# Optimization experiments

Measured on AMD Instinct MI355X. Metric: run time of the kernel, lower is better.

The kernel has to match this reference:

```python
import jax, jax.numpy as jnp
import numpy as np

IN, OUT, B = 2048, 1000, 8192
EXP = (2048, 4096, 6144, 8192)
LN_EPS = 1e-5


def _mish(v):
    return v * jnp.tanh(jax.nn.softplus(v))


def _gelu(v):
    return jax.nn.gelu(v, approximate=False)  # torch F.gelu default is exact erf


def setup_inputs() -> dict:
    key = jax.random.key(0)
    ks = iter(jax.random.split(key, 48))
    nk = lambda: next(ks)
    r = lambda shape, s=0.02: jax.random.normal(nk(), shape, jnp.float32) * s
    d = {"x": jax.random.normal(nk(), (B, IN), jnp.float32)}
    d["W"] = r((OUT, IN), 0.05)
    d["b"] = r((OUT,), 0.01)
    for i, e in enumerate(EXP):
        d[f"up_w{i}"] = r((e, IN))
        d[f"down_w{i}"] = r((OUT, e))
        d[f"router_w{i}"] = r((i + 2, IN), 0.05)
        d[f"router_b{i}"] = r((i + 2,), 0.01)
    d["scales"] = r((4,), 0.1)
    d["ln_g"] = jnp.ones((IN,), jnp.float32)
    d["ln_b"] = jnp.zeros((IN,), jnp.float32)
    d["dom_router_w"] = r((4, IN), 0.05)
    d["dom_router_b"] = r((4,), 0.01)
    d["dom_experts_w"] = r((OUT * 4, IN))
    d["calib_w"] = r((OUT, IN))
    d["calib_b"] = r((OUT,), 0.01)
    d["rg_w1"] = r((IN // 4, IN))
    d["rg_w2"] = r((OUT, IN // 4))
    d["rg_b2"] = r((OUT,), 0.01)
    d["zeta"] = jnp.float32(0.5)
    d["theta"] = jnp.float32(0.5)
    d["lambda_"] = jnp.float32(0.5)
    return d


def _forward(x, W, b,
             up_w0, down_w0, router_w0, router_b0,
             up_w1, down_w1, router_w1, router_b1,
             up_w2, down_w2, router_w2, router_b2,
             up_w3, down_w3, router_w3, router_b3,
             scales, ln_g, ln_b,
             dom_router_w, dom_router_b, dom_experts_w,
             calib_w, calib_b, rg_w1, rg_w2, rg_b2,
             zeta, theta, lambda_):
    acts = (jax.nn.silu, _gelu, _mish, jax.nn.relu)
    ups = (up_w0, up_w1, up_w2, up_w3)
    downs = (down_w0, down_w1, down_w2, down_w3)
    r_ws = (router_w0, router_w1, router_w2, router_w3)
    r_bs = (router_b0, router_b1, router_b2, router_b3)

    base_logits = x @ W.T + b                      # [B, OUT]
    # dropout is identity (eval mode)
    branch_outs = [acts[i](x @ ups[i].T) @ downs[i].T for i in range(4)]  # each [B, OUT]

    final_mix = base_logits
    for i in range(4):
        route = jax.nn.softmax(x @ r_ws[i].T + r_bs[i], axis=-1)  # [B, i+2]
        # only first i+1 routing weights are used (faithful to source)
        mix = sum(route[..., j:j + 1] * branch_outs[j] for j in range(i + 1))
        final_mix = final_mix + scales[i] * mix

    # pre_norm (LayerNorm, eps=1e-5)
    mu = jnp.mean(x, axis=-1, keepdims=True)
    var = jnp.var(x, axis=-1, keepdims=True)
    h = (x - mu) * jax.lax.rsqrt(var + LN_EPS) * ln_g + ln_b

    dom_logits = (jax.nn.silu(h) @ dom_experts_w.T).reshape(h.shape[0], 4, OUT)
    dom_w = jax.nn.softmax(h @ dom_router_w.T + dom_router_b, axis=-1)[..., None]  # [B,4,1]
    dom_mix = jnp.sum(dom_w * dom_logits, axis=-2)                                 # [B,OUT]

    calib = jnp.tanh(h @ calib_w.T + calib_b)
    reason = jnp.tanh(jax.nn.silu(x @ rg_w1.T) @ rg_w2.T + rg_b2)
    return final_mix + zeta * dom_mix + theta * calib + lambda_ * reason


def reference(x, W, b,
              up_w0, down_w0, router_w0, router_b0,
              up_w1, down_w1, router_w1, router_b1,
              up_w2, down_w2, router_w2, router_b2,
              up_w3, down_w3, router_w3, router_b3,
              scales, ln_g, ln_b,
              dom_router_w, dom_router_b, dom_experts_w,
              calib_w, calib_b, rg_w1, rg_w2, rg_b2,
              zeta, theta, lambda_):
    return _forward(x, W, b,
                    up_w0, down_w0, router_w0, router_b0,
                    up_w1, down_w1, router_w1, router_b1,
                    up_w2, down_w2, router_w2, router_b2,
                    up_w3, down_w3, router_w3, router_b3,
                    scales, ln_g, ln_b,
                    dom_router_w, dom_router_b, dom_experts_w,
                    calib_w, calib_b, rg_w1, rg_w2, rg_b2,
                    zeta, theta, lambda_)
```

## Files before the change

kernel.cpp:

```cpp
#include <hip/hip_runtime.h>
#include <hip/hip_bf16.h>
#include <cstdint>
#include <cstddef>

#define DEVI __device__ __forceinline__

typedef short bf16x8 __attribute__((ext_vector_type(8)));
typedef float f32x4 __attribute__((ext_vector_type(4)));

static constexpr int B_ = 8192;
static constexpr int IN_ = 2048;
static constexpr int OUT_ = 1000;

DEVI float bf2f(unsigned short u) { return __uint_as_float(((unsigned int)u) << 16); }
DEVI unsigned short f2bf(float f) {
    unsigned int x = __float_as_uint(f);
    unsigned int r = x + 0x7FFFu + ((x >> 16) & 1u);
    return (unsigned short)(r >> 16);
}

DEVI void gload16(const unsigned short* g, unsigned short* l) {
    __builtin_amdgcn_global_load_lds((const __attribute__((address_space(1))) void*)g,
                                     (__attribute__((address_space(3))) void*)l, 16, 0, 0);
}

DEVI void xcd_swizzle(int& bx, int& by) {
    const int NX = gridDim.x, NY = gridDim.y;
    if ((NY & 7) == 0) {
        const int NYc = NY >> 3;
        const int d = by * NX + bx;
        const int xcd = d & 7, idx = d >> 3;
        by = xcd * NYc + (idx % NYc);
        bx = idx / NYc;
    }
}

DEVI float fast_tanh(float x) {
    float xc = fminf(fmaxf(x, -10.f), 10.f);
    float e = __expf(2.f * xc);
    return 1.f - 2.f / (e + 1.f);
}

template <int ACT> DEVI float apply_act(float v) {
    if constexpr (ACT == 1) return v / (1.f + __expf(-v));
    else if constexpr (ACT == 2) return 0.5f * v * (1.f + erff(v * 0.70710678118654752f));
    else if constexpr (ACT == 3) {
        float p = __expf(fminf(v, 20.f));
        float sp = (v > 20.f) ? v : __logf(1.f + p);
        return v * fast_tanh(sp);
    } else if constexpr (ACT == 4) return fmaxf(v, 0.f);
    else if constexpr (ACT == 5) return fast_tanh(v);
    else return v;
}

__global__ __launch_bounds__(256) void cvt_kernel(const float* __restrict__ in,
                                                  unsigned short* __restrict__ out, int n4) {
    int stride = gridDim.x * blockDim.x;
    for (int i = blockIdx.x * blockDim.x + threadIdx.x; i < n4; i += stride) {
        float4 v = ((const float4*)in)[i];
        ushort4 o;
        o.x = f2bf(v.x); o.y = f2bf(v.y); o.z = f2bf(v.z); o.w = f2bf(v.w);
        ((ushort4*)out)[i] = o;
    }
}

__global__ __launch_bounds__(256) void cvt_dom_kernel(const float* __restrict__ in,
                                                      unsigned short* __restrict__ out) {
    const int total = 4096 * (IN_ / 4);
    int stride = gridDim.x * blockDim.x;
    for (int i = blockIdx.x * blockDim.x + threadIdx.x; i < total; i += stride) {
        int orow = i >> 9;
        int oc4 = i & 511;
        int s = orow >> 10, r = orow & 1023;
        ushort4 o = {0, 0, 0, 0};
        if (r < 1000) {
            float4 v = ((const float4*)(in + ((size_t)(s * 1000 + r)) * IN_))[oc4];
            o.x = f2bf(v.x); o.y = f2bf(v.y); o.z = f2bf(v.z); o.w = f2bf(v.w);
        }
        ((ushort4*)out)[i] = o;
    }
}

__global__ __launch_bounds__(256) void stats_kernel(const float* __restrict__ x,
                                                    const float* __restrict__ g,
                                                    const float* __restrict__ bta,
                                                    float* __restrict__ mu,
                                                    float* __restrict__ rstd,
                                                    unsigned short* __restrict__ xb,
                                                    unsigned short* __restrict__ hb,
                                                    unsigned short* __restrict__ shb,
                                                    const int wX, const int wH, const int wS) {
    const int r = blockIdx.x;
    const int t = threadIdx.x;
    const float* xr = x + (size_t)r * IN_;
    float v[8];
    float s = 0.f, q = 0.f;
#pragma unroll
    for (int i = 0; i < 8; ++i) {
        v[i] = xr[t + i * 256];
        s += v[i];
        q += v[i] * v[i];
    }
#pragma unroll
    for (int off = 32; off > 0; off >>= 1) {
        s += __shfl_down(s, off);
        q += __shfl_down(q, off);
    }
    __shared__ float ss[4], qq[4];
    if ((t & 63) == 0) { ss[t >> 6] = s; qq[t >> 6] = q; }
    __syncthreads();
    s = ss[0] + ss[1] + ss[2] + ss[3];
    q = qq[0] + qq[1] + qq[2] + qq[3];
    const float mean = s * (1.f / IN_);
    const float var = q * (1.f / IN_) - mean * mean;
    const float rs = rsqrtf(var + 1e-5f);
    if (t == 0) { mu[r] = mean; rstd[r] = rs; }
#pragma unroll
    for (int i = 0; i < 8; ++i) {
        int c = t + i * 256;
        if (wX) xb[(size_t)r * IN_ + c] = f2bf(v[i]);
        if (wH | wS) {
            float h = (v[i] - mean) * rs * g[c] + bta[c];
            if (wH) hb[(size_t)r * IN_ + c] = f2bf(h);
            if (wS) shb[(size_t)r * IN_ + c] = f2bf(h / (1.f + __expf(-h)));
        }
    }
}

__global__ __launch_bounds__(256) void router_kernel(
    const float* __restrict__ x, const float* __restrict__ mu, const float* __restrict__ rstd,
    const float* __restrict__ g, const float* __restrict__ bta,
    const float* __restrict__ rw0, const float* __restrict__ rb0,
    const float* __restrict__ rw1, const float* __restrict__ rb1,
    const float* __restrict__ rw2, const float* __restrict__ rb2,
    const float* __restrict__ rw3, const float* __restrict__ rb3,
    const float* __restrict__ scales, const float* __restrict__ domw,
    const float* __restrict__ domb, float* __restrict__ coeff) {
    const int r = blockIdx.x;
    const int t = threadIdx.x;
    __shared__ float xs[IN_];
    __shared__ float hs[IN_];
    __shared__ float dots[18];
    const float m = mu[r], rs = rstd[r];
#pragma unroll
    for (int i = 0; i < 8; ++i) {
        int c = t + i * 256;
        float xv = x[(size_t)r * IN_ + c];
        xs[c] = xv;
        hs[c] = (xv - m) * rs * g[c] + bta[c];
    }
    __syncthreads();
    const int w = t >> 6, l = t & 63;
    const float* wp[5] = {rw0, rw1, rw2, rw3, domw};
    for (int d = w; d < 18; d += 4) {
        int gidx, row;
        if (d < 2) { gidx = 0; row = d; }
        else if (d < 5) { gidx = 1; row = d - 2; }
        else if (d < 9) { gidx = 2; row = d - 5; }
        else if (d < 14) { gidx = 3; row = d - 9; }
        else { gidx = 4; row = d - 14; }
        const float* wt = wp[gidx] + (size_t)row * IN_;
        const float* src = (gidx == 4) ? hs : xs;
        float p = 0.f;
        for (int i = l; i < IN_; i += 64) p += src[i] * wt[i];
#pragma unroll
        for (int off = 32; off > 0; off >>= 1) p += __shfl_down(p, off);
        if (l == 0) dots[d] = p;
    }
    __syncthreads();
    if (t == 0) {
        const float* rbs[4] = {rb0, rb1, rb2, rb3};
        float c[4] = {0.f, 0.f, 0.f, 0.f};
        int off = 0;
        for (int i = 0; i < 4; ++i) {
            int n = i + 2;
            float lg[5], mx = -1e30f;
            for (int j = 0; j < n; ++j) { lg[j] = dots[off + j] + rbs[i][j]; mx = fmaxf(mx, lg[j]); }
            float den = 0.f;
            for (int j = 0; j < n; ++j) { lg[j] = expf(lg[j] - mx); den += lg[j]; }
            float inv = 1.f / den;
            float sci = scales[i];
            for (int j = 0; j <= i; ++j) c[j] += sci * lg[j] * inv;
            off += n;
        }
        float dl[4], mx = -1e30f;
        for (int k = 0; k < 4; ++k) { dl[k] = dots[14 + k] + domb[k]; mx = fmaxf(mx, dl[k]); }
        float den = 0.f;
        for (int k = 0; k < 4; ++k) { dl[k] = expf(dl[k] - mx); den += dl[k]; }
        float inv = 1.f / den;
        for (int j = 0; j < 4; ++j) coeff[(size_t)r * 8 + j] = c[j];
        for (int k = 0; k < 4; ++k) coeff[(size_t)r * 8 + 4 + k] = dl[k] * inv;
    }
}

__global__ __launch_bounds__(256) void dom_reduce(
    const unsigned short* __restrict__ U, const float* __restrict__ coeff,
    float* __restrict__ out, const float* __restrict__ zetap) {
    const float zeta = zetap[0];
    const int nGroups = B_ * (OUT_ / 8);
    const int stride = gridDim.x * blockDim.x;
    for (int i = blockIdx.x * blockDim.x + threadIdx.x; i < nGroups; i += stride) {
        const int r = i / 125;
        const int c8 = (i - r * 125) * 8;
        const float w0 = zeta * coeff[(size_t)r * 8 + 4];
        const float w1 = zeta * coeff[(size_t)r * 8 + 5];
        const float w2 = zeta * coeff[(size_t)r * 8 + 6];
        const float w3 = zeta * coeff[(size_t)r * 8 + 7];
        const unsigned short* ur = U + (size_t)r * 4096 + c8;
        bf16x8 p0 = *(const bf16x8*)(ur);
        bf16x8 p1 = *(const bf16x8*)(ur + 1024);
        bf16x8 p2 = *(const bf16x8*)(ur + 2048);
        bf16x8 p3 = *(const bf16x8*)(ur + 3072);
        float* orow = out + (size_t)r * OUT_ + c8;
#pragma unroll
        for (int j = 0; j < 8; ++j) {
            orow[j] += w0 * bf2f((unsigned short)p0[j]) + w1 * bf2f((unsigned short)p1[j]) +
                       w2 * bf2f((unsigned short)p2[j]) + w3 * bf2f((unsigned short)p3[j]);
        }
    }
}

template <int ACT>
__global__ __launch_bounds__(512, 2) void gemm8p(
    const unsigned short* __restrict__ A, const unsigned short* __restrict__ Bw,
    unsigned short* __restrict__ outB, const int N, const int K) {
    extern __shared__ unsigned short lds[];
    const int t = threadIdx.x;
    const int l = t & 63, w = t >> 6;
    const int wr = w >> 2, wc = w & 3;
    int bx = blockIdx.x, by = blockIdx.y;
    xcd_swizzle(bx, by);
    const int rowBase = by * 256, colBase = bx * 256;

    const int lr = l >> 3;
    const int lcs = (((l & 7) ^ lr) << 3);
    const unsigned short* aSrc[4];
    const unsigned short* bSrc[4];
    int aDst[4], bDst[4];
#pragma unroll
    for (int j = 0; j < 4; ++j) {
        const int h = j >> 1, ci = w * 2 + (j & 1);
        aSrc[j] = A + (size_t)(rowBase + h * 128 + ci * 8 + lr) * K + lcs;
        bSrc[j] = Bw + (size_t)(colBase + h * 128 + ci * 8 + lr) * K + lcs;
        aDst[j] = h * 8192 + ci * 512;
        bDst[j] = 16384 + h * 8192 + ci * 512;
    }

    const int fr = l & 15, fg = l >> 4;
    const int kx0 = ((fg ^ (fr & 7)) << 3);
    const int kx1 = (((4 + fg) ^ (fr & 7)) << 3);
    const int aRow = (wr * 128 + fr) * 64;
    const int bRow = 16384 + (wc * 64 + fr) * 64;

    f32x4 acc[8][4];
#pragma unroll
    for (int m = 0; m < 8; ++m)
#pragma unroll
        for (int n = 0; n < 4; ++n) acc[m][n] = (f32x4){0.f, 0.f, 0.f, 0.f};

    const int nt = K >> 6;

#pragma unroll
    for (int j = 0; j < 4; ++j) gload16(aSrc[j], &lds[aDst[j]]);
#pragma unroll
    for (int j = 0; j < 4; ++j) gload16(bSrc[j], &lds[bDst[j]]);

    bf16x8 aF[4][2], bF[2][2];

#define LOAD_A(mh)                                                                         \
    _Pragma("unroll") for (int m = 0; m < 4; ++m) {                                        \
        aF[m][0] = *(const bf16x8*)&lds[bo + aRow + ((mh)*64 + m * 16) * 64 + kx0];        \
        aF[m][1] = *(const bf16x8*)&lds[bo + aRow + ((mh)*64 + m * 16) * 64 + kx1];        \
    }
#define LOAD_B(nh)                                                                         \
    _Pragma("unroll") for (int n = 0; n < 2; ++n) {                                        \
        bF[n][0] = *(const bf16x8*)&lds[bo + bRow + ((nh)*32 + n * 16) * 64 + kx0];        \
        bF[n][1] = *(const bf16x8*)&lds[bo + bRow + ((nh)*32 + n * 16) * 64 + kx1];        \
    }
#define MFMA_PHASE(mh, nh)                                                                 \
    __builtin_amdgcn_s_setprio(1);                                                         \
    _Pragma("unroll") for (int m = 0; m < 4; ++m)                                          \
        _Pragma("unroll") for (int n = 0; n < 2; ++n) {                                    \
            acc[(mh)*4 + m][(nh)*2 + n] = __builtin_amdgcn_mfma_f32_16x16x32_bf16(         \
                aF[m][0], bF[n][0], acc[(mh)*4 + m][(nh)*2 + n], 0, 0, 0);                 \
            acc[(mh)*4 + m][(nh)*2 + n] = __builtin_amdgcn_mfma_f32_16x16x32_bf16(         \
                aF[m][1], bF[n][1], acc[(mh)*4 + m][(nh)*2 + n], 0, 0, 0);                 \
        }                                                                                  \
    __builtin_amdgcn_s_setprio(0);

    for (int ti = 0; ti < nt; ++ti) {
        const int bo = (ti & 1) << 15;
        const int so = bo ^ 32768;
        const int ko = (ti + 1) << 6;
        const bool pre = (ti + 1 < nt);
        asm volatile("s_waitcnt vmcnt(0)" ::: "memory");
        asm volatile("s_barrier" ::: "memory");
        if (pre) {
#pragma unroll
            for (int j = 0; j < 4; ++j) gload16(aSrc[j] + ko, &lds[so + aDst[j]]);
        }
        LOAD_A(0)
        LOAD_B(0)
        MFMA_PHASE(0, 0)
        asm volatile("s_barrier" ::: "memory");
        if (pre) {
#pragma unroll
            for (int j = 0; j < 4; ++j) gload16(bSrc[j] + ko, &lds[so + bDst[j]]);
        }
        LOAD_A(1)
        MFMA_PHASE(1, 0)
        asm volatile("s_barrier" ::: "memory");
        LOAD_B(1)
        MFMA_PHASE(1, 1)
        asm volatile("s_barrier" ::: "memory");
        LOAD_A(0)
        MFMA_PHASE(0, 1)
    }
#undef LOAD_A
#undef LOAD_B
#undef MFMA_PHASE

#pragma unroll
    for (int m = 0; m < 8; ++m) {
        const int grow0 = rowBase + wr * 128 + m * 16 + fg * 4;
#pragma unroll
        for (int n = 0; n < 4; ++n) {
            const int gcol = colBase + wc * 64 + n * 16 + fr;
#pragma unroll
            for (int j = 0; j < 4; ++j) {
                float v = apply_act<ACT>(acc[m][n][j]);
                outB[(size_t)(grow0 + j) * N + gcol] = f2bf(v);
            }
        }
    }
}

template <int ACT, int MODE, int BIASF>
__global__ __launch_bounds__(256) void gemm_lds(
    const unsigned short* __restrict__ A, const unsigned short* __restrict__ Bw,
    float* __restrict__ outF, unsigned short* __restrict__ outB,
    const float* __restrict__ bias, const float* __restrict__ coeff, const int cidx,
    const float* __restrict__ scalarp, const int N, const int K) {
    __shared__ unsigned short Asm[2][4096];
    __shared__ unsigned short Bsm[2][4096];
    const int t = threadIdx.x;
    const int l = t & 63;
    const int w = t >> 6;
    const int wr = w >> 1, wc = w & 1;
    int bx = blockIdx.x, by = blockIdx.y;
    xcd_swizzle(bx, by);
    const int rowBase = by * 128;
    const int colBase = bx * 128;

    const int lr = l >> 2;
    const int lk = (l & 3) << 3;
    const int ar0 = rowBase + w * 32 + lr;
    const int ar1 = ar0 + 16;
    int br0 = colBase + w * 32 + lr;      if (br0 >= N) br0 = N - 1;
    int br1 = colBase + w * 32 + 16 + lr; if (br1 >= N) br1 = N - 1;
    const unsigned short* pA0 = A + (size_t)ar0 * K + lk;
    const unsigned short* pA1 = A + (size_t)ar1 * K + lk;
    const unsigned short* pB0 = Bw + (size_t)br0 * K + lk;
    const unsigned short* pB1 = Bw + (size_t)br1 * K + lk;
    const int ldsA0 = (w * 32) * 32;
    const int ldsA1 = (w * 32 + 16) * 32;

    f32x4 acc[4][4];
#pragma unroll
    for (int m = 0; m < 4; ++m)
#pragma unroll
        for (int n = 0; n < 4; ++n) acc[m][n] = (f32x4){0.f, 0.f, 0.f, 0.f};

    const int nK = K >> 5;

    auto stage = [&](int buf, int kt) {
        const int ko = kt << 5;
        gload16(pA0 + ko, &Asm[buf][ldsA0]);
        gload16(pA1 + ko, &Asm[buf][ldsA1]);
        gload16(pB0 + ko, &Bsm[buf][ldsA0]);
        gload16(pB1 + ko, &Bsm[buf][ldsA1]);
    };

    stage(0, 0);
    __syncthreads();

    const int fr = l & 15;
    const int fg = l >> 4;
    const int aoff = (wr * 64 + fr) * 32 + fg * 8;
    const int boff = (wc * 64 + fr) * 32 + fg * 8;

    int buf = 0;
    for (int kt = 0; kt < nK; ++kt) {
        if (kt + 1 < nK) stage(buf ^ 1, kt + 1);
        bf16x8 af[4], bfr[4];
#pragma unroll
        for (int m = 0; m < 4; ++m) af[m] = *(const bf16x8*)&Asm[buf][aoff + m * 512];
#pragma unroll
        for (int n = 0; n < 4; ++n) bfr[n] = *(const bf16x8*)&Bsm[buf][boff + n * 512];
#pragma unroll
        for (int m = 0; m < 4; ++m)
#pragma unroll
            for (int n = 0; n < 4; ++n)
                acc[m][n] = __builtin_amdgcn_mfma_f32_16x16x32_bf16(af[m], bfr[n], acc[m][n], 0, 0, 0);
        __syncthreads();
        buf ^= 1;
    }

    const float scal = scalarp ? scalarp[0] : 1.0f;
#pragma unroll
    for (int m = 0; m < 4; ++m) {
        const int grow0 = rowBase + wr * 64 + m * 16 + fg * 4;
#pragma unroll
        for (int n = 0; n < 4; ++n) {
            const int gcol = colBase + wc * 64 + n * 16 + fr;
            if (gcol < N) {
                float bv = BIASF ? bias[gcol] : 0.f;
#pragma unroll
                for (int j = 0; j < 4; ++j) {
                    const int grow = grow0 + j;
                    float v = acc[m][n][j] + bv;
                    v = apply_act<ACT>(v);
                    float alpha = scal;
                    if (coeff) alpha *= coeff[(size_t)grow * 8 + cidx];
                    v *= alpha;
                    const size_t o = (size_t)grow * N + gcol;
                    if constexpr (MODE == 2) outB[o] = f2bf(v);
                    else if constexpr (MODE == 1) outF[o] += v;
                    else outF[o] = v;
                }
            }
        }
    }
}

template <int ASRC, int ASIL, int BSRC, int ACT, int OUTBF, int ACCUM, int BIASF>
__global__ __launch_bounds__(256) void gemm_bt(
    const void* __restrict__ Ap, const void* __restrict__ Bp,
    float* __restrict__ outF, unsigned short* __restrict__ outB,
    const float* __restrict__ bias, const float* __restrict__ coeff, const int cidx,
    const float* __restrict__ scalarp,
    const float* __restrict__ muP, const float* __restrict__ rsP,
    const float* __restrict__ lng, const float* __restrict__ lnb,
    const int N, const int K) {
    __shared__ unsigned short Asm[2][4096];
    __shared__ unsigned short Bsm[2][4096];
    const int t = threadIdx.x;
    const int l = t & 63;
    const int w = t >> 6;
    const int wr = w >> 1, wc = w & 1;
    int bx = blockIdx.x, by = blockIdx.y;
    xcd_swizzle(bx, by);
    const int rowBase = by * 128;
    const int colBase = bx * 128;

    const int srow = t >> 2;
    const int skol = (t & 3) << 3;
    const int arow0 = rowBase + srow;
    const int arow1 = arow0 + 64;
    int br0 = colBase + srow;        if (br0 >= N) br0 = N - 1;
    int br1 = colBase + srow + 64;   if (br1 >= N) br1 = N - 1;

    float mu0 = 0.f, rs0 = 1.f, mu1 = 0.f, rs1 = 1.f;
    if constexpr (ASRC == 2) {
        mu0 = muP[arow0]; rs0 = rsP[arow0];
        mu1 = muP[arow1]; rs1 = rsP[arow1];
    }

    auto ldA = [&](int row, float mu_, float rs_, int k0) -> bf16x8 {
        if constexpr (ASRC == 0) {
            bf16x8 v = *(const bf16x8*)((const unsigned short*)Ap + (size_t)row * K + k0);
            if constexpr (ASIL) {
                bf16x8 r;
#pragma unroll
                for (int i = 0; i < 8; ++i) {
                    float f = bf2f((unsigned short)v[i]);
                    r[i] = (short)f2bf(f / (1.f + __expf(-f)));
                }
                return r;
            }
            return v;
        } else {
            const float* f = (const float*)Ap + (size_t)row * K + k0;
            float4 v0 = *(const float4*)f;
            float4 v1 = *(const float4*)(f + 4);
            float vv[8] = {v0.x, v0.y, v0.z, v0.w, v1.x, v1.y, v1.z, v1.w};
            if constexpr (ASRC == 2) {
                float4 g0 = *(const float4*)(lng + k0), g1 = *(const float4*)(lng + k0 + 4);
                float4 b0 = *(const float4*)(lnb + k0), b1 = *(const float4*)(lnb + k0 + 4);
                float gg[8] = {g0.x, g0.y, g0.z, g0.w, g1.x, g1.y, g1.z, g1.w};
                float bb[8] = {b0.x, b0.y, b0.z, b0.w, b1.x, b1.y, b1.z, b1.w};
#pragma unroll
                for (int i = 0; i < 8; ++i) vv[i] = (vv[i] - mu_) * rs_ * gg[i] + bb[i];
            }
            if constexpr (ASIL) {
#pragma unroll
                for (int i = 0; i < 8; ++i) vv[i] = vv[i] / (1.f + __expf(-vv[i]));
            }
            bf16x8 r;
#pragma unroll
            for (int i = 0; i < 8; ++i) r[i] = (short)f2bf(vv[i]);
            return r;
        }
    };
    auto ldB = [&](int row, int k0) -> bf16x8 {
        if constexpr (BSRC == 0) {
            return *(const bf16x8*)((const unsigned short*)Bp + (size_t)row * K + k0);
        } else {
            const float* f = (const float*)Bp + (size_t)row * K + k0;
            float4 v0 = *(const float4*)f;
            float4 v1 = *(const float4*)(f + 4);
            float vv[8] = {v0.x, v0.y, v0.z, v0.w, v1.x, v1.y, v1.z, v1.w};
            bf16x8 r;
#pragma unroll
            for (int i = 0; i < 8; ++i) r[i] = (short)f2bf(vv[i]);
            return r;
        }
    };

    const int wo = t * 8;

    f32x4 acc[4][4];
#pragma unroll
    for (int m = 0; m < 4; ++m)
#pragma unroll
        for (int n = 0; n < 4; ++n) acc[m][n] = (f32x4){0.f, 0.f, 0.f, 0.f};

    const int nK = K >> 5;

    bf16x8 a0 = ldA(arow0, mu0, rs0, skol);
    bf16x8 a1 = ldA(arow1, mu1, rs1, skol);
    bf16x8 b0 = ldB(br0, skol);
    bf16x8 b1 = ldB(br1, skol);
    *(bf16x8*)&Asm[0][wo] = a0; *(bf16x8*)&Asm[0][wo + 2048] = a1;
    *(bf16x8*)&Bsm[0][wo] = b0; *(bf16x8*)&Bsm[0][wo + 2048] = b1;
    __syncthreads();

    const int fr = l & 15;
    const int fg = l >> 4;
    const int aoff = (wr * 64 + fr) * 32 + fg * 8;
    const int boff = (wc * 64 + fr) * 32 + fg * 8;

    for (int kt = 0; kt < nK; ++kt) {
        const int cur = kt & 1;
        if (kt + 1 < nK) {
            const int ko = ((kt + 1) << 5) + skol;
            a0 = ldA(arow0, mu0, rs0, ko);
            a1 = ldA(arow1, mu1, rs1, ko);
            b0 = ldB(br0, ko);
            b1 = ldB(br1, ko);
        }
        bf16x8 af[4], bfr[4];
#pragma unroll
        for (int m = 0; m < 4; ++m) af[m] = *(const bf16x8*)&Asm[cur][aoff + m * 512];
#pragma unroll
        for (int n = 0; n < 4; ++n) bfr[n] = *(const bf16x8*)&Bsm[cur][boff + n * 512];
#pragma unroll
        for (int m = 0; m < 4; ++m)
#pragma unroll
            for (int n = 0; n < 4; ++n)
                acc[m][n] = __builtin_amdgcn_mfma_f32_16x16x32_bf16(af[m], bfr[n], acc[m][n], 0, 0, 0);
        if (kt + 1 < nK) {
            __syncthreads();
            const int nxt = cur ^ 1;
            *(bf16x8*)&Asm[nxt][wo] = a0; *(bf16x8*)&Asm[nxt][wo + 2048] = a1;
            *(bf16x8*)&Bsm[nxt][wo] = b0; *(bf16x8*)&Bsm[nxt][wo + 2048] = b1;
            __syncthreads();
        }
    }

    const float scal = scalarp ? scalarp[0] : 1.0f;
#pragma unroll
    for (int m = 0; m < 4; ++m) {
        const int grow0 = rowBase + wr * 64 + m * 16 + fg * 4;
#pragma unroll
        for (int n = 0; n < 4; ++n) {
            const int gcol = colBase + wc * 64 + n * 16 + fr;
            if (gcol < N) {
                float bv = BIASF ? bias[gcol] : 0.f;
#pragma unroll
                for (int j = 0; j < 4; ++j) {
                    const int grow = grow0 + j;
                    float v = acc[m][n][j] + bv;
                    v = apply_act<ACT>(v);
                    float alpha = scal;
                    if (coeff) alpha *= coeff[(size_t)grow * 8 + cidx];
                    v *= alpha;
                    const size_t o = (size_t)grow * N + gcol;
                    if (OUTBF) outB[o] = f2bf(v);
                    else if (ACCUM) outF[o] += v;
                    else outF[o] = v;
                }
            }
        }
    }
}

static inline void cvt(const float* in, unsigned short* out, size_t n, hipStream_t s) {
    int n4 = (int)(n >> 2);
    int blocks = (n4 + 255) / 256;
    if (blocks > 4096) blocks = 4096;
    cvt_kernel<<<blocks, 256, 0, s>>>(in, out, n4);
}

extern "C" void kernel_launch(void* const* d_in, const int* in_sizes, int n_in,
                              void* d_out, int out_size, void* d_ws, size_t ws_size,
                              hipStream_t stream) {
    (void)in_sizes; (void)n_in; (void)out_size;
    const float* x = (const float*)d_in[0];
    const float* W = (const float*)d_in[1];
    const float* bvec = (const float*)d_in[2];
    const float* up_w[4] = {(const float*)d_in[3], (const float*)d_in[7], (const float*)d_in[11], (const float*)d_in[15]};
    const float* down_w[4] = {(const float*)d_in[4], (const float*)d_in[8], (const float*)d_in[12], (const float*)d_in[16]};
    const float* r_w[4] = {(const float*)d_in[5], (const float*)d_in[9], (const float*)d_in[13], (const float*)d_in[17]};
    const float* r_b[4] = {(const float*)d_in[6], (const float*)d_in[10], (const float*)d_in[14], (const float*)d_in[18]};
    const float* scales = (const float*)d_in[19];
    const float* ln_g = (const float*)d_in[20];
    const float* ln_b = (const float*)d_in[21];
    const float* dom_rw = (const float*)d_in[22];
    const float* dom_rb = (const float*)d_in[23];
    const float* dom_ew = (const float*)d_in[24];
    const float* cal_w = (const float*)d_in[25];
    const float* cal_b = (const float*)d_in[26];
    const float* rg_w1 = (const float*)d_in[27];
    const float* rg_w2 = (const float*)d_in[28];
    const float* rg_b2 = (const float*)d_in[29];
    const float* zeta = (const float*)d_in[30];
    const float* theta = (const float*)d_in[31];
    const float* lam = (const float*)d_in[32];
    float* out = (float*)d_out;

    const int E[4] = {2048, 4096, 6144, 8192};
    auto al = [](size_t v) { return (v + 255) & ~(size_t)255; };

    size_t fastNeed = al((size_t)B_ * 8 * 4) + 2 * al((size_t)B_ * 4) +
                      2 * al((size_t)B_ * IN_ * 2) +
                      al((size_t)OUT_ * IN_ * 2) +
                      al((size_t)4096 * IN_ * 2) +
                      al((size_t)OUT_ * IN_ * 2) +
                      al((size_t)512 * IN_ * 2) + al((size_t)OUT_ * 512 * 2) +
                      al((size_t)B_ * 8192 * 2) + al((size_t)B_ * 512 * 2);
    for (int j = 0; j < 4; ++j)
        fastNeed += al((size_t)E[j] * IN_ * 2) + al((size_t)OUT_ * E[j] * 2);

    char* p = (char*)d_ws;
    auto alloc = [&](size_t bytes) { char* r = p; p += (bytes + 255) & ~(size_t)255; return r; };

    const int NT_OUT = (OUT_ + 127) / 128;
    const int MT = B_ / 128;

    if (ws_size >= fastNeed) {
        float* coeff = (float*)alloc((size_t)B_ * 8 * 4);
        float* muP = (float*)alloc((size_t)B_ * 4);
        float* rsP = (float*)alloc((size_t)B_ * 4);
        unsigned short* xb = (unsigned short*)alloc((size_t)B_ * IN_ * 2);
        unsigned short* shb = (unsigned short*)alloc((size_t)B_ * IN_ * 2);
        unsigned short* Wb = (unsigned short*)alloc((size_t)OUT_ * IN_ * 2);
        unsigned short* domN = (unsigned short*)alloc((size_t)4096 * IN_ * 2);
        unsigned short* calb = (unsigned short*)alloc((size_t)OUT_ * IN_ * 2);
        unsigned short* rg1b = (unsigned short*)alloc((size_t)512 * IN_ * 2);
        unsigned short* rg2b = (unsigned short*)alloc((size_t)OUT_ * 512 * 2);
        unsigned short* U = (unsigned short*)alloc((size_t)B_ * 8192 * 2);
        unsigned short* T = (unsigned short*)alloc((size_t)B_ * 512 * 2);
        unsigned short* upb[4];
        unsigned short* downb[4];
        for (int j = 0; j < 4; ++j) {
            upb[j] = (unsigned short*)alloc((size_t)E[j] * IN_ * 2);
            downb[j] = (unsigned short*)alloc((size_t)OUT_ * E[j] * 2);
        }
        unsigned short* hbU = U;

        hipFuncSetAttribute((const void*)gemm8p<1>, hipFuncAttributeMaxDynamicSharedMemorySize, 131072);
        hipFuncSetAttribute((const void*)gemm8p<2>, hipFuncAttributeMaxDynamicSharedMemorySize, 131072);
        hipFuncSetAttribute((const void*)gemm8p<3>, hipFuncAttributeMaxDynamicSharedMemorySize, 131072);
        hipFuncSetAttribute((const void*)gemm8p<4>, hipFuncAttributeMaxDynamicSharedMemorySize, 131072);

        cvt(W, Wb, (size_t)OUT_ * IN_, stream);
        cvt_dom_kernel<<<4096, 256, 0, stream>>>(dom_ew, domN);
        cvt(cal_w, calb, (size_t)OUT_ * IN_, stream);
        cvt(rg_w1, rg1b, (size_t)512 * IN_, stream);
        cvt(rg_w2, rg2b, (size_t)OUT_ * 512, stream);
        for (int j = 0; j < 4; ++j) {
            cvt(up_w[j], upb[j], (size_t)E[j] * IN_, stream);
            cvt(down_w[j], downb[j], (size_t)OUT_ * E[j], stream);
        }

        stats_kernel<<<B_, 256, 0, stream>>>(x, ln_g, ln_b, muP, rsP, xb, hbU, shb, 1, 1, 1);
        router_kernel<<<B_, 256, 0, stream>>>(x, muP, rsP, ln_g, ln_b,
                                              r_w[0], r_b[0], r_w[1], r_b[1], r_w[2], r_b[2],
                                              r_w[3], r_b[3], scales, dom_rw, dom_rb, coeff);

        gemm_lds<0, 0, 1><<<dim3(NT_OUT, MT), 256, 0, stream>>>(
            xb, Wb, out, nullptr, bvec, nullptr, 0, nullptr, OUT_, IN_);

        gemm_lds<5, 1, 1><<<dim3(NT_OUT, MT), 256, 0, stream>>>(
            hbU, calb, out, nullptr, cal_b, nullptr, 0, theta, OUT_, IN_);

        gemm_lds<0, 2, 0><<<dim3(32, MT), 256, 0, stream>>>(
            shb, domN, nullptr, U, nullptr, nullptr, 0, nullptr, 4096, IN_);
        dom_reduce<<<2048, 256, 0, stream>>>(U, coeff, out, zeta);

        gemm8p<1><<<dim3(E[0] / 256, B_ / 256), 512, 131072, stream>>>(xb, upb[0], U, E[0], IN_);
        gemm_lds<0, 1, 0><<<dim3(NT_OUT, MT), 256, 0, stream>>>(
            U, downb[0], out, nullptr, nullptr, coeff, 0, nullptr, OUT_, E[0]);
        gemm8p<2><<<dim3(E[1] / 256, B_ / 256), 512, 131072, stream>>>(xb, upb[1], U, E[1], IN_);
        gemm_lds<0, 1, 0><<<dim3(NT_OUT, MT), 256, 0, stream>>>(
            U, downb[1], out, nullptr, nullptr, coeff, 1, nullptr, OUT_, E[1]);
        gemm8p<3><<<dim3(E[2] / 256, B_ / 256), 512, 131072, stream>>>(xb, upb[2], U, E[2], IN_);
        gemm_lds<0, 1, 0><<<dim3(NT_OUT, MT), 256, 0, stream>>>(
            U, downb[2], out, nullptr, nullptr, coeff, 2, nullptr, OUT_, E[2]);
        gemm8p<4><<<dim3(E[3] / 256, B_ / 256), 512, 131072, stream>>>(xb, upb[3], U, E[3], IN_);
        gemm_lds<0, 1, 0><<<dim3(NT_OUT, MT), 256, 0, stream>>>(
            U, downb[3], out, nullptr, nullptr, coeff, 3, nullptr, OUT_, E[3]);

        gemm_lds<1, 2, 0><<<dim3(4, MT), 256, 0, stream>>>(
            xb, rg1b, nullptr, T, nullptr, nullptr, 0, nullptr, 512, IN_);
        gemm_lds<5, 1, 1><<<dim3(NT_OUT, MT), 256, 0, stream>>>(
            T, rg2b, out, nullptr, rg_b2, nullptr, 0, lam, OUT_, 512);
        return;
    }

    const size_t S_coeff = al((size_t)B_ * 8 * 4);
    const size_t S_mu = al((size_t)B_ * 4);
    const size_t S_act = al((size_t)B_ * IN_ * 2);
    size_t S_W = al((size_t)OUT_ * IN_ * 2) + al((size_t)4 * OUT_ * IN_ * 2) +
                 al((size_t)OUT_ * IN_ * 2) + al((size_t)512 * IN_ * 2) + al((size_t)OUT_ * 512 * 2);
    for (int j = 0; j < 4; ++j) S_W += al((size_t)E[j] * IN_ * 2) + al((size_t)OUT_ * E[j] * 2);

    auto needOf = [&](bool bfl, bool cwl, int ch) {
        size_t n = S_coeff + 2 * S_mu;
        if (bfl) n += 3 * S_act;
        if (cwl) n += S_W;
        n += al((size_t)ch * 8192 * 2) + al((size_t)ch * 512 * 2);
        return n;
    };
    bool bf = false, cw = false;
    int CH = 512;
    {
        const bool cb[7] = {true, true, true, true, true, true, false};
        const bool cc[7] = {true, true, true, false, false, false, false};
        const int  cch[7] = {8192, 4096, 2048, 4096, 2048, 512, 512};
        for (int i = 0; i < 7; ++i) {
            if (needOf(cb[i], cc[i], cch[i]) <= ws_size || i == 6) {
                bf = cb[i]; cw = cc[i]; CH = cch[i];
                break;
            }
        }
    }

    float* coeff = (float*)alloc((size_t)B_ * 8 * 4);
    float* muP = (float*)alloc((size_t)B_ * 4);
    float* rsP = (float*)alloc((size_t)B_ * 4);
    unsigned short *xb = nullptr, *hb = nullptr, *shb = nullptr;
    if (bf) {
        xb = (unsigned short*)alloc((size_t)B_ * IN_ * 2);
        hb = (unsigned short*)alloc((size_t)B_ * IN_ * 2);
        shb = (unsigned short*)alloc((size_t)B_ * IN_ * 2);
    }
    unsigned short *Wb = nullptr, *upb[4] = {}, *downb[4] = {}, *domb_ = nullptr,
                   *calb = nullptr, *rg1b = nullptr, *rg2b = nullptr;
    if (cw) {
        Wb = (unsigned short*)alloc((size_t)OUT_ * IN_ * 2);
        domb_ = (unsigned short*)alloc((size_t)4 * OUT_ * IN_ * 2);
        calb = (unsigned short*)alloc((size_t)OUT_ * IN_ * 2);
        rg1b = (unsigned short*)alloc((size_t)512 * IN_ * 2);
        rg2b = (unsigned short*)alloc((size_t)OUT_ * 512 * 2);
        for (int j = 0; j < 4; ++j) {
            upb[j] = (unsigned short*)alloc((size_t)E[j] * IN_ * 2);
            downb[j] = (unsigned short*)alloc((size_t)OUT_ * E[j] * 2);
        }
    }
    unsigned short* U = (unsigned short*)alloc((size_t)CH * 8192 * 2);
    unsigned short* T = (unsigned short*)alloc((size_t)CH * 512 * 2);

    if (cw) {
        cvt(W, Wb, (size_t)OUT_ * IN_, stream);
        for (int j = 0; j < 4; ++j) {
            cvt(up_w[j], upb[j], (size_t)E[j] * IN_, stream);
            cvt(down_w[j], downb[j], (size_t)OUT_ * E[j], stream);
        }
        cvt(dom_ew, domb_, (size_t)4 * OUT_ * IN_, stream);
        cvt(cal_w, calb, (size_t)OUT_ * IN_, stream);
        cvt(rg_w1, rg1b, (size_t)512 * IN_, stream);
        cvt(rg_w2, rg2b, (size_t)OUT_ * 512, stream);
    }

    stats_kernel<<<B_, 256, 0, stream>>>(x, ln_g, ln_b, muP, rsP, xb, hb, shb,
                                         bf ? 1 : 0, bf ? 1 : 0, bf ? 1 : 0);
    router_kernel<<<B_, 256, 0, stream>>>(x, muP, rsP, ln_g, ln_b,
                                          r_w[0], r_b[0], r_w[1], r_b[1], r_w[2], r_b[2],
                                          r_w[3], r_b[3], scales, dom_rw, dom_rb, coeff);

#define GARG(A, BW, OF, OB, BI, CF, CI, SC, MU, NN, KK) \
    (const void*)(A), (const void*)(BW), OF, OB, BI, CF, CI, SC, MU, rsP, ln_g, ln_b, NN, KK
#define LX(ACT, OUTBF, ACCUM, BIASF, GRID, Abf, Af, Bb, Bf, OF, OB, BI, CF, CI, SC, MU, NN, KK)         \
    do {                                                                                                \
        if (bf) {                                                                                       \
            if (cw) gemm_bt<0, 0, 0, ACT, OUTBF, ACCUM, BIASF><<<GRID, 256, 0, stream>>>(               \
                GARG(Abf, Bb, OF, OB, BI, CF, CI, SC, MU, NN, KK));                                     \
            else gemm_bt<0, 0, 1, ACT, OUTBF, ACCUM, BIASF><<<GRID, 256, 0, stream>>>(                  \
                GARG(Abf, Bf, OF, OB, BI, CF, CI, SC, MU, NN, KK));                                     \
        } else gemm_bt<1, 0, 1, ACT, OUTBF, ACCUM, BIASF><<<GRID, 256, 0, stream>>>(                    \
                GARG(Af, Bf, OF, OB, BI, CF, CI, SC, MU, NN, KK));                                      \
    } while (0)
#define LD(ACT, OUTBF, ACCUM, BIASF, GRID, A, Bb, Bf, OF, OB, BI, CF, CI, SC, NN, KK)                   \
    do {                                                                                                \
        if (cw) gemm_bt<0, 0, 0, ACT, OUTBF, ACCUM, BIASF><<<GRID, 256, 0, stream>>>(                   \
            GARG(A, Bb, OF, OB, BI, CF, CI, SC, muP, NN, KK));                                          \
        else gemm_bt<0, 0, 1, ACT, OUTBF, ACCUM, BIASF><<<GRID, 256, 0, stream>>>(                      \
            GARG(A, Bf, OF, OB, BI, CF, CI, SC, muP, NN, KK));                                          \
    } while (0)

    LX(0, 0, 0, 1, dim3(NT_OUT, MT), xb, x, Wb, W, out, nullptr, bvec, (const float*)nullptr, 0,
       (const float*)nullptr, muP, OUT_, IN_);

    for (int k = 0; k < 4; ++k) {
        const unsigned short* Bb = cw ? domb_ + (size_t)k * OUT_ * IN_ : nullptr;
        const float* Bf = dom_ew + (size_t)k * OUT_ * IN_;
        if (bf) {
            if (cw) gemm_bt<0, 0, 0, 0, 0, 1, 0><<<dim3(NT_OUT, MT), 256, 0, stream>>>(
                GARG(shb, Bb, out, nullptr, nullptr, coeff, 4 + k, zeta, muP, OUT_, IN_));
            else gemm_bt<0, 0, 1, 0, 0, 1, 0><<<dim3(NT_OUT, MT), 256, 0, stream>>>(
                GARG(shb, Bf, out, nullptr, nullptr, coeff, 4 + k, zeta, muP, OUT_, IN_));
        } else {
            gemm_bt<2, 1, 1, 0, 0, 1, 0><<<dim3(NT_OUT, MT), 256, 0, stream>>>(
                GARG(x, Bf, out, nullptr, nullptr, coeff, 4 + k, zeta, muP, OUT_, IN_));
        }
    }

    if (bf) {
        if (cw) gemm_bt<0, 0, 0, 5, 0, 1, 1><<<dim3(NT_OUT, MT), 256, 0, stream>>>(
            GARG(hb, calb, out, nullptr, cal_b, nullptr, 0, theta, muP, OUT_, IN_));
        else gemm_bt<0, 0, 1, 5, 0, 1, 1><<<dim3(NT_OUT, MT), 256, 0, stream>>>(
            GARG(hb, cal_w, out, nullptr, cal_b, nullptr, 0, theta, muP, OUT_, IN_));
    } else {
        gemm_bt<2, 0, 1, 5, 0, 1, 1><<<dim3(NT_OUT, MT), 256, 0, stream>>>(
            GARG(x, cal_w, out, nullptr, cal_b, nullptr, 0, theta, muP, OUT_, IN_));
    }

    for (int r0 = 0; r0 < B_; r0 += CH) {
        const int MTC = CH / 128;
        const unsigned short* xbC = bf ? xb + (size_t)r0 * IN_ : nullptr;
        const float* xC = x + (size_t)r0 * IN_;
        float* outC = out + (size_t)r0 * OUT_;
        const float* coeffC = coeff + (size_t)r0 * 8;
        for (int j = 0; j < 4; ++j) {
            dim3 gu(E[j] / 128, MTC);
            if (j == 0)
                LX(1, 1, 0, 0, gu, xbC, xC, upb[0], up_w[0], nullptr, U, nullptr, (const float*)nullptr, 0,
                   (const float*)nullptr, muP, E[0], IN_);
            else if (j == 1)
                LX(2, 1, 0, 0, gu, xbC, xC, upb[1], up_w[1], nullptr, U, nullptr, (const float*)nullptr, 0,
                   (const float*)nullptr, muP, E[1], IN_);
            else if (j == 2)
                LX(3, 1, 0, 0, gu, xbC, xC, upb[2], up_w[2], nullptr, U, nullptr, (const float*)nullptr, 0,
                   (const float*)nullptr, muP, E[2], IN_);
            else
                LX(4, 1, 0, 0, gu, xbC, xC, upb[3], up_w[3], nullptr, U, nullptr, (const float*)nullptr, 0,
                   (const float*)nullptr, muP, E[3], IN_);
            LD(0, 0, 1, 0, dim3(NT_OUT, MTC), U, downb[j], down_w[j], outC, nullptr, nullptr,
               coeffC, j, (const float*)nullptr, OUT_, E[j]);
        }
        LX(1, 1, 0, 0, dim3(4, MTC), xbC, xC, rg1b, rg_w1, nullptr, T, nullptr, (const float*)nullptr, 0,
           (const float*)nullptr, muP, 512, IN_);
        LD(5, 0, 1, 1, dim3(NT_OUT, MTC), T, rg2b, rg_w2, outC, nullptr, rg_b2, nullptr, 0, lam, OUT_, 512);
    }
#undef LX
#undef LD
#undef GARG
}
```

Baseline: 2.049 ms.

## Double K-tile depth to 64 with XOR-swizzled LDS layout in 128x128 GEMM

Result: faster. 1.910 ms, median of 2 (-6.8%).

```diff
diff --git a/kernel.cpp b/kernel.cpp
--- a/kernel.cpp
+++ b/kernel.cpp
@@ -336,13 +336,13 @@
 }
 
 template <int ACT, int MODE, int BIASF>
-__global__ __launch_bounds__(256) void gemm_lds(
+__global__ __launch_bounds__(256) void gemm_bk64(
     const unsigned short* __restrict__ A, const unsigned short* __restrict__ Bw,
     float* __restrict__ outF, unsigned short* __restrict__ outB,
     const float* __restrict__ bias, const float* __restrict__ coeff, const int cidx,
     const float* __restrict__ scalarp, const int N, const int K) {
-    __shared__ unsigned short Asm[2][4096];
-    __shared__ unsigned short Bsm[2][4096];
+    __shared__ unsigned short Asm[2][8192];
+    __shared__ unsigned short Bsm[2][8192];
     const int t = threadIdx.x;
     const int l = t & 63;
     const int w = t >> 6;
@@ -352,18 +352,20 @@
     const int rowBase = by * 128;
     const int colBase = bx * 128;
 
-    const int lr = l >> 2;
-    const int lk = (l & 3) << 3;
-    const int ar0 = rowBase + w * 32 + lr;
-    const int ar1 = ar0 + 16;
-    int br0 = colBase + w * 32 + lr;      if (br0 >= N) br0 = N - 1;
-    int br1 = colBase + w * 32 + 16 + lr; if (br1 >= N) br1 = N - 1;
-    const unsigned short* pA0 = A + (size_t)ar0 * K + lk;
-    const unsigned short* pA1 = A + (size_t)ar1 * K + lk;
-    const unsigned short* pB0 = Bw + (size_t)br0 * K + lk;
-    const unsigned short* pB1 = Bw + (size_t)br1 * K + lk;
-    const int ldsA0 = (w * 32) * 32;
-    const int ldsA1 = (w * 32 + 16) * 32;
+    const int lr = l >> 3;
+    const int lcs = (((l & 7) ^ lr) << 3);
+    const unsigned short* aS[4];
+    const unsigned short* bS[4];
+    int dst[4];
+#pragma unroll
+    for (int i = 0; i < 4; ++i) {
+        const int r0 = w * 32 + i * 8;
+        const int ar = rowBase + r0 + lr;
+        int br = colBase + r0 + lr; if (br >= N) br = N - 1;
+        aS[i] = A + (size_t)ar * K + lcs;
+        bS[i] = Bw + (size_t)br * K + lcs;
+        dst[i] = r0 * 64;
+    }
 
     f32x4 acc[4][4];
 #pragma unroll
@@ -371,14 +373,14 @@
 #pragma unroll
         for (int n = 0; n < 4; ++n) acc[m][n] = (f32x4){0.f, 0.f, 0.f, 0.f};
 
-    const int nK = K >> 5;
+    const int nK = K >> 6;
 
     auto stage = [&](int buf, int kt) {
-        const int ko = kt << 5;
-        gload16(pA0 + ko, &Asm[buf][ldsA0]);
-        gload16(pA1 + ko, &Asm[buf][ldsA1]);
-        gload16(pB0 + ko, &Bsm[buf][ldsA0]);
-        gload16(pB1 + ko, &Bsm[buf][ldsA1]);
+        const int ko = kt << 6;
+#pragma unroll
+        for (int i = 0; i < 4; ++i) gload16(aS[i] + ko, &Asm[buf][dst[i]]);
+#pragma unroll
+        for (int i = 0; i < 4; ++i) gload16(bS[i] + ko, &Bsm[buf][dst[i]]);
     };
 
     stage(0, 0);
@@ -386,22 +388,32 @@
 
     const int fr = l & 15;
     const int fg = l >> 4;
-    const int aoff = (wr * 64 + fr) * 32 + fg * 8;
-    const int boff = (wc * 64 + fr) * 32 + fg * 8;
+    const int kx0 = ((fg ^ (fr & 7)) << 3);
+    const int kx1 = (((4 + fg) ^ (fr & 7)) << 3);
 
     int buf = 0;
     for (int kt = 0; kt < nK; ++kt) {
         if (kt + 1 < nK) stage(buf ^ 1, kt + 1);
-        bf16x8 af[4], bfr[4];
-#pragma unroll
-        for (int m = 0; m < 4; ++m) af[m] = *(const bf16x8*)&Asm[buf][aoff + m * 512];
-#pragma unroll
-        for (int n = 0; n < 4; ++n) bfr[n] = *(const bf16x8*)&Bsm[buf][boff + n * 512];
+        bf16x8 af[4][2], bfr[4][2];
+#pragma unroll
+        for (int m = 0; m < 4; ++m) {
+            const int ar = (wr * 64 + m * 16 + fr) * 64;
+            af[m][0] = *(const bf16x8*)&Asm[buf][ar + kx0];
+            af[m][1] = *(const bf16x8*)&Asm[buf][ar + kx1];
+        }
+#pragma unroll
+        for (int n = 0; n < 4; ++n) {
+            const int br = (wc * 64 + n * 16 + fr) * 64;
+            bfr[n][0] = *(const bf16x8*)&Bsm[buf][br + kx0];
+            bfr[n][1] = *(const bf16x8*)&Bsm[buf][br + kx1];
+        }
 #pragma unroll
         for (int m = 0; m < 4; ++m)
 #pragma unroll
-            for (int n = 0; n < 4; ++n)
-                acc[m][n] = __builtin_amdgcn_mfma_f32_16x16x32_bf16(af[m], bfr[n], acc[m][n], 0, 0, 0);
+            for (int n = 0; n < 4; ++n) {
+                acc[m][n] = __builtin_amdgcn_mfma_f32_16x16x32_bf16(af[m][0], bfr[n][0], acc[m][n], 0, 0, 0);
+                acc[m][n] = __builtin_amdgcn_mfma_f32_16x16x32_bf16(af[m][1], bfr[n][1], acc[m][n], 0, 0, 0);
+            }
         __syncthreads();
         buf ^= 1;
     }
@@ -689,32 +701,32 @@
                                               r_w[0], r_b[0], r_w[1], r_b[1], r_w[2], r_b[2],
                                               r_w[3], r_b[3], scales, dom_rw, dom_rb, coeff);
 
-        gemm_lds<0, 0, 1><<<dim3(NT_OUT, MT), 256, 0, stream>>>(
+        gemm_bk64<0, 0, 1><<<dim3(NT_OUT, MT), 256, 0, stream>>>(
             xb, Wb, out, nullptr, bvec, nullptr, 0, nullptr, OUT_, IN_);
 
-        gemm_lds<5, 1, 1><<<dim3(NT_OUT, MT), 256, 0, stream>>>(
+        gemm_bk64<5, 1, 1><<<dim3(NT_OUT, MT), 256, 0, stream>>>(
             hbU, calb, out, nullptr, cal_b, nullptr, 0, theta, OUT_, IN_);
 
-        gemm_lds<0, 2, 0><<<dim3(32, MT), 256, 0, stream>>>(
+        gemm_bk64<0, 2, 0><<<dim3(32, MT), 256, 0, stream>>>(
             shb, domN, nullptr, U, nullptr, nullptr, 0, nullptr, 4096, IN_);
         dom_reduce<<<2048, 256, 0, stream>>>(U, coeff, out, zeta);
 
         gemm8p<1><<<dim3(E[0] / 256, B_ / 256), 512, 131072, stream>>>(xb, upb[0], U, E[0], IN_);
-        gemm_lds<0, 1, 0><<<dim3(NT_OUT, MT), 256, 0, stream>>>(
+        gemm_bk64<0, 1, 0><<<dim3(NT_OUT, MT), 256, 0, stream>>>(
             U, downb[0], out, nullptr, nullptr, coeff, 0, nullptr, OUT_, E[0]);
         gemm8p<2><<<dim3(E[1] / 256, B_ / 256), 512, 131072, stream>>>(xb, upb[1], U, E[1], IN_);
-        gemm_lds<0, 1, 0><<<dim3(NT_OUT, MT), 256, 0, stream>>>(
+        gemm_bk64<0, 1, 0><<<dim3(NT_OUT, MT), 256, 0, stream>>>(
             U, downb[1], out, nullptr, nullptr, coeff, 1, nullptr, OUT_, E[1]);
         gemm8p<3><<<dim3(E[2] / 256, B_ / 256), 512, 131072, stream>>>(xb, upb[2], U, E[2], IN_);
-        gemm_lds<0, 1, 0><<<dim3(NT_OUT, MT), 256, 0, stream>>>(
+        gemm_bk64<0, 1, 0><<<dim3(NT_OUT, MT), 256, 0, stream>>>(
             U, downb[2], out, nullptr, nullptr, coeff, 2, nullptr, OUT_, E[2]);
         gemm8p<4><<<dim3(E[3] / 256, B_ / 256), 512, 131072, stream>>>(xb, upb[3], U, E[3], IN_);
-        gemm_lds<0, 1, 0><<<dim3(NT_OUT, MT), 256, 0, stream>>>(
+        gemm_bk64<0, 1, 0><<<dim3(NT_OUT, MT), 256, 0, stream>>>(
             U, downb[3], out, nullptr, nullptr, coeff, 3, nullptr, OUT_, E[3]);
 
-        gemm_lds<1, 2, 0><<<dim3(4, MT), 256, 0, stream>>>(
+        gemm_bk64<1, 2, 0><<<dim3(4, MT), 256, 0, stream>>>(
             xb, rg1b, nullptr, T, nullptr, nullptr, 0, nullptr, 512, IN_);
-        gemm_lds<5, 1, 1><<<dim3(NT_OUT, MT), 256, 0, stream>>>(
+        gemm_bk64<5, 1, 1><<<dim3(NT_OUT, MT), 256, 0, stream>>>(
             T, rg2b, out, nullptr, rg_b2, nullptr, 0, lam, OUT_, 512);
         return;
     }
```
